# Kernel tuning notes

Hardware: AMD Instinct MI355X
Metric: run time of the kernel (lower is better)

## Reference

```python
import jax, jax.numpy as jnp
import numpy as np

N_NODES = 100000
N_EDGES = 1600000
F_IN = 128
HEADS = 4
C_OUT = 32
NEG_SLOPE = 0.2


def setup_inputs() -> dict:
    key = jax.random.key(0)
    k1, k2, k3, k4, k5, k6 = jax.random.split(key, 6)
    x = jax.random.normal(k1, (N_NODES, F_IN), dtype=jnp.float32)
    edge_index = jax.random.randint(k2, (2, N_EDGES), 0, N_NODES, dtype=jnp.int64)
    # glorot-ish scales
    W = jax.random.normal(k3, (F_IN, HEADS * C_OUT), dtype=jnp.float32) * (1.0 / np.sqrt(F_IN))
    att_src = jax.random.normal(k4, (HEADS, C_OUT), dtype=jnp.float32) * (1.0 / np.sqrt(C_OUT))
    att_dst = jax.random.normal(k5, (HEADS, C_OUT), dtype=jnp.float32) * (1.0 / np.sqrt(C_OUT))
    bias = jnp.zeros((HEADS * C_OUT,), dtype=jnp.float32)
    return {"x": x, "edge_index": edge_index, "W": W,
            "att_src": att_src, "att_dst": att_dst, "bias": bias}


def _gat_forward(x, edge_index, W, att_src, att_dst, bias):
    N = x.shape[0]
    H, C = att_src.shape
    h = (x @ W).reshape(N, H, C)                      # [N,H,C]
    # PyG GATConv default: add self-loops
    loops = jnp.arange(N, dtype=edge_index.dtype)
    src = jnp.concatenate([edge_index[0], loops])     # [E+N]
    dst = jnp.concatenate([edge_index[1], loops])
    a_src = jnp.einsum("nhc,hc->nh", h, att_src)      # [N,H]
    a_dst = jnp.einsum("nhc,hc->nh", h, att_dst)
    e = jax.nn.leaky_relu(a_src[src] + a_dst[dst], NEG_SLOPE)  # [E+N,H]
    # segment softmax over destination node (every node has a self-loop)
    m = jax.ops.segment_max(e, dst, num_segments=N)
    e = jnp.exp(e - m[dst])
    s = jax.ops.segment_sum(e, dst, num_segments=N)
    alpha = e / (s[dst] + 1e-16)                      # [E+N,H]
    msg = h[src] * alpha[:, :, None]                  # [E+N,H,C]
    out = jax.ops.segment_sum(msg, dst, num_segments=N).reshape(N, H * C)
    return jnp.tanh(out + bias)


def reference(x, edge_index, W, att_src, att_dst, bias):
    return _gat_forward(x, edge_index, W, att_src, att_dst, bias)
```

## Files before the change

kernel.cpp:

```cpp
#include <hip/hip_runtime.h>
#include <math.h>

#define NN 100000
#define NE 1600000
#define F_IN 128
#define HEADS 4
#define HC 128
#define NEG_SLOPE 0.2f
#define NBKT 391
#define BCAP 5120

typedef __attribute__((ext_vector_type(8))) short bf16x8;
typedef __attribute__((ext_vector_type(4))) float f32x4;

static __device__ __forceinline__ short f2bf_rne(float f) {
    unsigned u = __float_as_uint(f);
    unsigned r = (u + 0x7FFFu + ((u >> 16) & 1u)) >> 16;
    return (short)r;
}
static __device__ __forceinline__ float bf2f(short s) {
    return __uint_as_float(((unsigned)(unsigned short)s) << 16);
}

__global__ __launch_bounds__(256) void prep_kernel(
        const float* __restrict__ W, short* __restrict__ wt_hi, short* __restrict__ wt_lo,
        const int* __restrict__ ei, int* __restrict__ flag, int* __restrict__ bcur) {
    if (blockIdx.x == 0 && threadIdx.x < 64) {
        int l = threadIdx.x;
        int v = ei[2 * l + 1];
        for (int off = 1; off < 64; off <<= 1) v |= __shfl_xor(v, off);
        if (l == 0) *flag = (v == 0) ? 1 : 0;
    }
    if (blockIdx.x == 1 || blockIdx.x == 2) {
        int z = (blockIdx.x - 1) * 256 + threadIdx.x;
        if (z < NBKT) bcur[z] = 0;
    }
    int i = blockIdx.x * 256 + threadIdx.x;
    if (i >= F_IN * HC) return;
    int k = i >> 7, n = i & 127;
    float f = W[k * HC + n];
    short hb = f2bf_rne(f);
    wt_hi[n * F_IN + k] = hb;
    wt_lo[n * F_IN + k] = f2bf_rne(f - bf2f(hb));
}

__global__ __launch_bounds__(256) void mfma_gemm_kernel(
        const float* __restrict__ x, const short* __restrict__ wt_hi,
        const short* __restrict__ wt_lo, const float* __restrict__ att_src,
        const float* __restrict__ att_dst, unsigned short* __restrict__ h_bf,
        float* __restrict__ a_src, float* __restrict__ a_dst) {
    int strip = (blockIdx.x * 256 + threadIdx.x) >> 6;
    int lane = threadIdx.x & 63;
    if (strip >= NN / 16) return;
    int l15 = lane & 15;
    int q = lane >> 4;

    f32x4 acc[8];
#pragma unroll
    for (int nt = 0; nt < 8; ++nt) acc[nt] = (f32x4){0.f, 0.f, 0.f, 0.f};

    const float* xp = x + (size_t)(strip * 16 + l15) * F_IN + q * 8;

#pragma unroll
    for (int ki = 0; ki < 4; ++ki) {
        float4 v0 = *(const float4*)(xp + ki * 32);
        float4 v1 = *(const float4*)(xp + ki * 32 + 4);
        float vv[8] = {v0.x, v0.y, v0.z, v0.w, v1.x, v1.y, v1.z, v1.w};
        bf16x8 a_hi, a_lo;
#pragma unroll
        for (int j = 0; j < 8; ++j) {
            short hb = f2bf_rne(vv[j]);
            a_hi[j] = hb;
            a_lo[j] = f2bf_rne(vv[j] - bf2f(hb));
        }
        int koff = ki * 32 + q * 8;
#pragma unroll
        for (int nt = 0; nt < 8; ++nt) {
            int widx = (nt * 16 + l15) * F_IN + koff;
            bf16x8 b_hi = *(const bf16x8*)(wt_hi + widx);
            bf16x8 b_lo = *(const bf16x8*)(wt_lo + widx);
            acc[nt] = __builtin_amdgcn_mfma_f32_16x16x32_bf16(a_hi, b_hi, acc[nt], 0, 0, 0);
            acc[nt] = __builtin_amdgcn_mfma_f32_16x16x32_bf16(a_lo, b_hi, acc[nt], 0, 0, 0);
            acc[nt] = __builtin_amdgcn_mfma_f32_16x16x32_bf16(a_hi, b_lo, acc[nt], 0, 0, 0);
        }
    }

    int orow = strip * 16 + q * 4;
#pragma unroll
    for (int nt = 0; nt < 8; ++nt)
#pragma unroll
        for (int r = 0; r < 4; ++r)
            h_bf[(size_t)(orow + r) * HC + nt * 16 + l15] =
                (unsigned short)f2bf_rne(acc[nt][r]);

    float as0[4], as1[4], ad0[4], ad1[4];
#pragma unroll
    for (int hd = 0; hd < 4; ++hd) {
        as0[hd] = att_src[hd * 32 + l15];
        as1[hd] = att_src[hd * 32 + 16 + l15];
        ad0[hd] = att_dst[hd * 32 + l15];
        ad1[hd] = att_dst[hd * 32 + 16 + l15];
    }
#pragma unroll
    for (int r = 0; r < 4; ++r) {
#pragma unroll
        for (int hd = 0; hd < 4; ++hd) {
            float ps = acc[2 * hd][r] * as0[hd] + acc[2 * hd + 1][r] * as1[hd];
            float pd = acc[2 * hd][r] * ad0[hd] + acc[2 * hd + 1][r] * ad1[hd];
#pragma unroll
            for (int off = 1; off < 16; off <<= 1) {
                ps += __shfl_xor(ps, off);
                pd += __shfl_xor(pd, off);
            }
            if (l15 == 0) {
                int row = orow + r;
                a_src[row * 4 + hd] = ps;
                a_dst[row * 4 + hd] = pd;
            }
        }
    }
}

__global__ __launch_bounds__(256) void bucket_scatter_kernel(
        const int* __restrict__ ei, const int* __restrict__ flag,
        int* __restrict__ bcur, unsigned* __restrict__ pairs) {
    __shared__ int lhist[NBKT];
    __shared__ int gbase[NBKT];
    int t = threadIdx.x;
    for (int i = t; i < NBKT; i += 256) lhist[i] = 0;
    __syncthreads();
    int is64 = *flag;
    int base = blockIdx.x * 4096;

    unsigned wrd[16];
    int meta[16];
#pragma unroll
    for (int it = 0; it < 16; ++it) {
        int e = base + it * 256 + t;
        if (e < NE) {
            int src = is64 ? ei[2 * e] : ei[e];
            int dst = is64 ? ei[2 * NE + 2 * e] : ei[NE + e];
            int b = dst >> 8;
            int r = atomicAdd(&lhist[b], 1);
            wrd[it] = (unsigned)src | ((unsigned)(dst & 255) << 17);
            meta[it] = b | (r << 9);
        } else {
            meta[it] = -1;
        }
    }
    __syncthreads();
    for (int i = t; i < NBKT; i += 256)
        gbase[i] = lhist[i] ? atomicAdd(&bcur[i], lhist[i]) : 0;
    __syncthreads();
#pragma unroll
    for (int it = 0; it < 16; ++it) {
        if (meta[it] >= 0) {
            int b = meta[it] & 511;
            int r = meta[it] >> 9;
            pairs[(size_t)b * BCAP + gbase[b] + r] = wrd[it];
        }
    }
}

__global__ __launch_bounds__(256) void bucket_csr_kernel(
        const int* __restrict__ bcur, const unsigned* __restrict__ pairs,
        const float* __restrict__ a_src, const float* __restrict__ a_dst,
        int* __restrict__ deg, int* __restrict__ offsets,
        int* __restrict__ csr_src, unsigned* __restrict__ wal,
        float2* __restrict__ selfdata) {
    __shared__ unsigned lpairs[BCAP];
    __shared__ int sd[256];
    __shared__ int cnt256[256];
    __shared__ int lcur[256];
    __shared__ float sumw[1024];

    int b = blockIdx.x;
    int t = threadIdx.x;
    int node = (b << 8) + t;

    int partial = 0;
    for (int i = t; i < b; i += 256) partial += bcur[i];
    sd[t] = partial;
    __syncthreads();
    for (int off = 128; off > 0; off >>= 1) {
        if (t < off) sd[t] += sd[t + off];
        __syncthreads();
    }
    int bktbase = sd[0];
    __syncthreads();

    cnt256[t] = 0;
    for (int i = t; i < 1024; i += 256) sumw[i] = 0.f;
    __syncthreads();

    int cnt = bcur[b];
    const unsigned* __restrict__ bp = pairs + (size_t)b * BCAP;
    for (int i = t; i < cnt; i += 256) {
        unsigned w = bp[i];
        lpairs[i] = w;
        atomicAdd(&cnt256[w >> 17], 1);
    }
    __syncthreads();

    int v = cnt256[t];
    sd[t] = v;
    __syncthreads();
    for (int off = 1; off < 256; off <<= 1) {
        int u = (t >= off) ? sd[t - off] : 0;
        __syncthreads();
        sd[t] += u;
        __syncthreads();
    }
    int myoff = bktbase + sd[t] - v;
    if (node < NN) {
        deg[node] = v;
        offsets[node] = myoff;
    }
    lcur[t] = myoff;
    __syncthreads();

    for (int i = t; i < cnt; i += 256) {
        unsigned w = lpairs[i];
        int src = (int)(w & 0x1FFFFu);
        int dl = (int)(w >> 17);
        float4 as = ((const float4*)a_src)[src];
        float4 ad = ((const float4*)a_dst)[(b << 8) + dl];
        float e0 = as.x + ad.x; e0 = (e0 < 0.f) ? NEG_SLOPE * e0 : e0;
        float e1 = as.y + ad.y; e1 = (e1 < 0.f) ? NEG_SLOPE * e1 : e1;
        float e2 = as.z + ad.z; e2 = (e2 < 0.f) ? NEG_SLOPE * e2 : e2;
        float e3 = as.w + ad.w; e3 = (e3 < 0.f) ? NEG_SLOPE * e3 : e3;
        float w0 = __expf(e0), w1 = __expf(e1), w2 = __expf(e2), w3 = __expf(e3);
        int pos = atomicAdd(&lcur[dl], 1);
        csr_src[pos] = src;
        unsigned lo = (unsigned)(unsigned short)f2bf_rne(w0) |
                      ((unsigned)(unsigned short)f2bf_rne(w1) << 16);
        unsigned hi = (unsigned)(unsigned short)f2bf_rne(w2) |
                      ((unsigned)(unsigned short)f2bf_rne(w3) << 16);
        ((uint2*)wal)[pos] = make_uint2(lo, hi);
        atomicAdd(&sumw[dl * 4 + 0], w0);
        atomicAdd(&sumw[dl * 4 + 1], w1);
        atomicAdd(&sumw[dl * 4 + 2], w2);
        atomicAdd(&sumw[dl * 4 + 3], w3);
    }
    __syncthreads();

    if (node < NN) {
        float4 as = ((const float4*)a_src)[node];
        float4 ad = ((const float4*)a_dst)[node];
        float sf[4];
        float e0 = as.x + ad.x; e0 = (e0 < 0.f) ? NEG_SLOPE * e0 : e0; sf[0] = __expf(e0);
        float e1 = as.y + ad.y; e1 = (e1 < 0.f) ? NEG_SLOPE * e1 : e1; sf[1] = __expf(e1);
        float e2 = as.z + ad.z; e2 = (e2 < 0.f) ? NEG_SLOPE * e2 : e2; sf[2] = __expf(e2);
        float e3 = as.w + ad.w; e3 = (e3 < 0.f) ? NEG_SLOPE * e3 : e3; sf[3] = __expf(e3);
#pragma unroll
        for (int hd = 0; hd < 4; ++hd) {
            float tot = sumw[t * 4 + hd] + sf[hd];
            float inv = 1.f / (tot + 1e-16f);
            selfdata[node * 4 + hd] = make_float2(inv, sf[hd] * inv);
        }
    }
}

__global__ __launch_bounds__(256) void gat_aggr_kernel(
        const int* __restrict__ offsets, const int* __restrict__ deg,
        const int* __restrict__ csr_src, const unsigned* __restrict__ wal,
        const float2* __restrict__ selfdata,
        const unsigned* __restrict__ h2, const float* __restrict__ bias,
        float* __restrict__ out) {
    int wid = (blockIdx.x * 256 + threadIdx.x) >> 6;
    int dst = __builtin_amdgcn_readfirstlane(wid);
    if (dst >= NN) return;
    int lane = threadIdx.x & 63;
    int hd = lane >> 4;
    unsigned hsel2 = (unsigned)(hd & 2);
    unsigned hsel1 = (unsigned)(hd & 1);

    int start = offsets[dst];
    int n = deg[dst];
    float2 sdta = selfdata[dst * 4 + hd];

    float accx = 0.f, accy = 0.f;
    int j = 0;
    for (; j + 3 < n; j += 4) {
        int base = start + j;
        int s0 = csr_src[base + 0];
        int s1 = csr_src[base + 1];
        int s2 = csr_src[base + 2];
        int s3 = csr_src[base + 3];
        uint2 wv0 = ((const uint2*)wal)[base + 0];
        uint2 wv1 = ((const uint2*)wal)[base + 1];
        uint2 wv2 = ((const uint2*)wal)[base + 2];
        uint2 wv3 = ((const uint2*)wal)[base + 3];
        unsigned u0 = h2[(size_t)s0 * 64 + lane];
        unsigned u1 = h2[(size_t)s1 * 64 + lane];
        unsigned u2 = h2[(size_t)s2 * 64 + lane];
        unsigned u3 = h2[(size_t)s3 * 64 + lane];
        unsigned ws0 = hsel2 ? wv0.y : wv0.x;
        unsigned ws1 = hsel2 ? wv1.y : wv1.x;
        unsigned ws2 = hsel2 ? wv2.y : wv2.x;
        unsigned ws3 = hsel2 ? wv3.y : wv3.x;
        float w0 = __uint_as_float(hsel1 ? (ws0 & 0xFFFF0000u) : (ws0 << 16));
        float w1 = __uint_as_float(hsel1 ? (ws1 & 0xFFFF0000u) : (ws1 << 16));
        float w2 = __uint_as_float(hsel1 ? (ws2 & 0xFFFF0000u) : (ws2 << 16));
        float w3 = __uint_as_float(hsel1 ? (ws3 & 0xFFFF0000u) : (ws3 << 16));
        accx += w0 * __uint_as_float(u0 << 16);
        accy += w0 * __uint_as_float(u0 & 0xFFFF0000u);
        accx += w1 * __uint_as_float(u1 << 16);
        accy += w1 * __uint_as_float(u1 & 0xFFFF0000u);
        accx += w2 * __uint_as_float(u2 << 16);
        accy += w2 * __uint_as_float(u2 & 0xFFFF0000u);
        accx += w3 * __uint_as_float(u3 << 16);
        accy += w3 * __uint_as_float(u3 & 0xFFFF0000u);
    }
    for (; j < n; ++j) {
        int base = start + j;
        int s0 = csr_src[base];
        uint2 wv0 = ((const uint2*)wal)[base];
        unsigned u0 = h2[(size_t)s0 * 64 + lane];
        unsigned ws0 = hsel2 ? wv0.y : wv0.x;
        float w0 = __uint_as_float(hsel1 ? (ws0 & 0xFFFF0000u) : (ws0 << 16));
        accx += w0 * __uint_as_float(u0 << 16);
        accy += w0 * __uint_as_float(u0 & 0xFFFF0000u);
    }

    unsigned us = h2[(size_t)dst * 64 + lane];
    float2 b2 = ((const float2*)bias)[lane];
    float ox = tanhf(accx * sdta.x + sdta.y * __uint_as_float(us << 16) + b2.x);
    float oy = tanhf(accy * sdta.x + sdta.y * __uint_as_float(us & 0xFFFF0000u) + b2.y);
    ((float2*)out)[(size_t)dst * 64 + lane] = make_float2(ox, oy);
}

extern "C" void kernel_launch(void* const* d_in, const int* in_sizes, int n_in,
                              void* d_out, int out_size, void* d_ws, size_t ws_size,
                              hipStream_t stream) {
    const float* x       = (const float*)d_in[0];
    const int*   ei      = (const int*)  d_in[1];
    const float* W       = (const float*)d_in[2];
    const float* att_src = (const float*)d_in[3];
    const float* att_dst = (const float*)d_in[4];
    const float* bias    = (const float*)d_in[5];
    float* out = (float*)d_out;

    unsigned short* h_bf = (unsigned short*)d_ws;
    float* a_src = (float*)(h_bf + (size_t)NN * HC);
    float* a_dst = a_src + (size_t)NN * HEADS;
    short* wt_hi = (short*)(a_dst + (size_t)NN * HEADS);
    short* wt_lo = wt_hi + F_IN * HC;
    int* flag    = (int*)(wt_lo + F_IN * HC);
    int* bcur    = flag + 4;
    int* deg     = bcur + NBKT + 1;
    int* offsets = deg + NN;
    int* csr_src = offsets + NN;
    unsigned* wal = (unsigned*)(csr_src + NE);
    float2* selfdata = (float2*)(wal + (size_t)NE * 2);
    unsigned* pairs = (unsigned*)(selfdata + (size_t)NN * HEADS);

    hipLaunchKernelGGL(prep_kernel, dim3(64), dim3(256), 0, stream,
                       W, wt_hi, wt_lo, ei, flag, bcur);

    hipLaunchKernelGGL(bucket_scatter_kernel, dim3((NE + 4095) / 4096), dim3(256), 0, stream,
                       ei, flag, bcur, pairs);

    hipLaunchKernelGGL(mfma_gemm_kernel, dim3((NN / 16 + 3) / 4), dim3(256), 0, stream,
                       x, wt_hi, wt_lo, att_src, att_dst, h_bf, a_src, a_dst);

    hipLaunchKernelGGL(bucket_csr_kernel, dim3(NBKT), dim3(256), 0, stream,
                       bcur, pairs, a_src, a_dst, deg, offsets, csr_src, wal, selfdata);

    hipLaunchKernelGGL(gat_aggr_kernel, dim3(NN * 64 / 256), dim3(256), 0, stream,
                       offsets, deg, csr_src, wal, selfdata,
                       (const unsigned*)h_bf, bias, out);
}
```

Baseline: 315.3 us.

## Stage split weight tiles in LDS and halve GEMM output columns per block

The GEMM kernel now splits the 128 output columns into two halves across blocks. Each block first copies its 64-column half of the bf16 hi/lo transposed weights into padded shared memory, then its MFMA loop reads B operands from LDS instead of global memory. This removes the repeated global weight reads per wave and halves accumulator registers, which may raise occupancy. In exchange, the x rows are read and split into hi/lo twice (once per column half), and there is a block-wide sync plus an LDS fill per block.

```diff
diff --git a/kernel.cpp b/kernel.cpp
--- a/kernel.cpp
+++ b/kernel.cpp
@@ -9,6 +9,7 @@
 #define NEG_SLOPE 0.2f
 #define NBKT 391
 #define BCAP 5120
+#define LDK 136
 
 typedef __attribute__((ext_vector_type(8))) short bf16x8;
 typedef __attribute__((ext_vector_type(4))) float f32x4;
@@ -49,15 +50,31 @@
         const short* __restrict__ wt_lo, const float* __restrict__ att_src,
         const float* __restrict__ att_dst, unsigned short* __restrict__ h_bf,
         float* __restrict__ a_src, float* __restrict__ a_dst) {
-    int strip = (blockIdx.x * 256 + threadIdx.x) >> 6;
-    int lane = threadIdx.x & 63;
+    __shared__ short lw_hi[64 * LDK];
+    __shared__ short lw_lo[64 * LDK];
+    int t = threadIdx.x;
+    int nh = blockIdx.x & 1;
+    int blk = blockIdx.x >> 1;
+
+    for (int c = t; c < 1024; c += 256) {
+        int n = c >> 4;
+        int kk = (c & 15) * 8;
+        bf16x8 vh = *(const bf16x8*)(wt_hi + (nh * 64 + n) * F_IN + kk);
+        bf16x8 vl = *(const bf16x8*)(wt_lo + (nh * 64 + n) * F_IN + kk);
+        *(bf16x8*)(lw_hi + n * LDK + kk) = vh;
+        *(bf16x8*)(lw_lo + n * LDK + kk) = vl;
+    }
+    __syncthreads();
+
+    int strip = blk * 4 + (t >> 6);
     if (strip >= NN / 16) return;
+    int lane = t & 63;
     int l15 = lane & 15;
     int q = lane >> 4;
 
-    f32x4 acc[8];
-#pragma unroll
-    for (int nt = 0; nt < 8; ++nt) acc[nt] = (f32x4){0.f, 0.f, 0.f, 0.f};
+    f32x4 acc[4];
+#pragma unroll
+    for (int nt = 0; nt < 4; ++nt) acc[nt] = (f32x4){0.f, 0.f, 0.f, 0.f};
 
     const float* xp = x + (size_t)(strip * 16 + l15) * F_IN + q * 8;
 
@@ -75,10 +92,10 @@
         }
         int koff = ki * 32 + q * 8;
 #pragma unroll
-        for (int nt = 0; nt < 8; ++nt) {
-            int widx = (nt * 16 + l15) * F_IN + koff;
-            bf16x8 b_hi = *(const bf16x8*)(wt_hi + widx);
-            bf16x8 b_lo = *(const bf16x8*)(wt_lo + widx);
+        for (int nt = 0; nt < 4; ++nt) {
+            int lidx = (nt * 16 + l15) * LDK + koff;
+            bf16x8 b_hi = *(const bf16x8*)(lw_hi + lidx);
+            bf16x8 b_lo = *(const bf16x8*)(lw_lo + lidx);
             acc[nt] = __builtin_amdgcn_mfma_f32_16x16x32_bf16(a_hi, b_hi, acc[nt], 0, 0, 0);
             acc[nt] = __builtin_amdgcn_mfma_f32_16x16x32_bf16(a_lo, b_hi, acc[nt], 0, 0, 0);
             acc[nt] = __builtin_amdgcn_mfma_f32_16x16x32_bf16(a_hi, b_lo, acc[nt], 0, 0, 0);
@@ -86,27 +103,25 @@
     }
 
     int orow = strip * 16 + q * 4;
-#pragma unroll
-    for (int nt = 0; nt < 8; ++nt)
+    int cbase = nh * 64;
+#pragma unroll
+    for (int nt = 0; nt < 4; ++nt)
 #pragma unroll
         for (int r = 0; r < 4; ++r)
-            h_bf[(size_t)(orow + r) * HC + nt * 16 + l15] =
+            h_bf[(size_t)(orow + r) * HC + cbase + nt * 16 + l15] =
                 (unsigned short)f2bf_rne(acc[nt][r]);
 
-    float as0[4], as1[4], ad0[4], ad1[4];
-#pragma unroll
-    for (int hd = 0; hd < 4; ++hd) {
-        as0[hd] = att_src[hd * 32 + l15];
-        as1[hd] = att_src[hd * 32 + 16 + l15];
-        ad0[hd] = att_dst[hd * 32 + l15];
-        ad1[hd] = att_dst[hd * 32 + 16 + l15];
-    }
-#pragma unroll
-    for (int r = 0; r < 4; ++r) {
-#pragma unroll
-        for (int hd = 0; hd < 4; ++hd) {
-            float ps = acc[2 * hd][r] * as0[hd] + acc[2 * hd + 1][r] * as1[hd];
-            float pd = acc[2 * hd][r] * ad0[hd] + acc[2 * hd + 1][r] * ad1[hd];
+#pragma unroll
+    for (int hl = 0; hl < 2; ++hl) {
+        int hd = nh * 2 + hl;
+        float as0 = att_src[hd * 32 + l15];
+        float as1 = att_src[hd * 32 + 16 + l15];
+        float ad0 = att_dst[hd * 32 + l15];
+        float ad1 = att_dst[hd * 32 + 16 + l15];
+#pragma unroll
+        for (int r = 0; r < 4; ++r) {
+            float ps = acc[2 * hl][r] * as0 + acc[2 * hl + 1][r] * as1;
+            float pd = acc[2 * hl][r] * ad0 + acc[2 * hl + 1][r] * ad1;
 #pragma unroll
             for (int off = 1; off < 16; off <<= 1) {
                 ps += __shfl_xor(ps, off);
@@ -361,7 +376,7 @@
     hipLaunchKernelGGL(bucket_scatter_kernel, dim3((NE + 4095) / 4096), dim3(256), 0, stream,
                        ei, flag, bcur, pairs);
 
-    hipLaunchKernelGGL(mfma_gemm_kernel, dim3((NN / 16 + 3) / 4), dim3(256), 0, stream,
+    hipLaunchKernelGGL(mfma_gemm_kernel, dim3(1563 * 2), dim3(256), 0, stream,
                        x, wt_hi, wt_lo, att_src, att_dst, h_bf, a_src, a_dst);
 
     hipLaunchKernelGGL(bucket_csr_kernel, dim3(NBKT), dim3(256), 0, stream,
```

Result: faster. 279.0 us (-11.5%).
